# Optimization experiments

Measured on AMD Instinct MI355X. Metric: run time of the kernel, lower is better.

Reference implementation:

```python
import jax, jax.numpy as jnp
import numpy as np


def setup_inputs() -> dict:
    key = jax.random.key(0)
    k1, k2, k3 = jax.random.split(key, 3)
    N, E, D = 100000, 3200000, 32  # neurons, total edges (fan-in sum), feature dim
    src = jax.random.normal(k1, (N, D), dtype=jnp.float32)
    gather_idx = jax.random.randint(k2, (E,), 0, N, dtype=jnp.int32)
    # repeat_interleave(arange(N), repeats) is nondecreasing -> sorted segment ids
    segment_ids = jnp.sort(jax.random.randint(k3, (E,), 0, N, dtype=jnp.int32))
    return {"src": src, "gather_idx": gather_idx, "segment_ids": segment_ids, "num_segments": N}


def reference(src, gather_idx, segment_ids, num_segments):
    # gather neuron input values: [E, D]
    gathered = src[gather_idx]
    # scatter_mean over variable-length groups (segment mean)
    sums = jax.ops.segment_sum(gathered, segment_ids, num_segments=num_segments,
                               indices_are_sorted=True)
    counts = jax.ops.segment_sum(jnp.ones((gathered.shape[0],), dtype=src.dtype),
                                 segment_ids, num_segments=num_segments,
                                 indices_are_sorted=True)
    return sums / jnp.maximum(counts, 1.0)[:, None]
```

## Files before the change

kernel.cpp:

```cpp
#include <hip/hip_runtime.h>
#include <hip/hip_fp16.h>


constexpr int D = 32;
constexpr int GSZ = 4;
constexpr int BLOCK = 256;
constexpr int SEGS_PER_BLOCK = BLOCK / GSZ;

typedef _Float16 half8 __attribute__((ext_vector_type(8)));

__global__ __launch_bounds__(BLOCK) void prep_kernel(
    const float* __restrict__ src,
    const int*   __restrict__ segid,
    int*         __restrict__ start,
    _Float16*    __restrict__ hsrc,
    int E, int N, int total)
{
    const int e = blockIdx.x * BLOCK + threadIdx.x;

    if (e <= E) {
        int s, p;
        if (e == E) { s = N; p = segid[E - 1]; }
        else        { s = segid[e]; p = (e == 0) ? -1 : segid[e - 1]; }
        for (int n = p + 1; n <= s; ++n) start[n] = e;
    }

    const int i = e * 8;
    if (i < total) {
        const float4 a = *(const float4*)(src + i);
        const float4 b = *(const float4*)(src + i + 4);
        half8 h;
        h[0] = (_Float16)a.x; h[1] = (_Float16)a.y;
        h[2] = (_Float16)a.z; h[3] = (_Float16)a.w;
        h[4] = (_Float16)b.x; h[5] = (_Float16)b.y;
        h[6] = (_Float16)b.z; h[7] = (_Float16)b.w;
        *(half8*)(hsrc + i) = h;
    }
}

__global__ __launch_bounds__(BLOCK) void AggregationLayer_53051436040325_kernel(
    const _Float16* __restrict__ hsrc,
    const int*      __restrict__ gidx,
    const int*      __restrict__ start,
    float*          __restrict__ out,
    int N)
{
    const int n   = blockIdx.x * SEGS_PER_BLOCK + (threadIdx.x >> 2);
    const int sub = threadIdx.x & (GSZ - 1);
    if (n >= N) return;

    const int lo = start[n];
    const int hi = start[n + 1];

    const _Float16* sp = hsrc + sub * 8;

    float acc[8];
#pragma unroll
    for (int j = 0; j < 8; ++j) acc[j] = 0.f;

    int e = lo;
    for (; e + 8 <= hi; e += 8) {
        int g[8];
#pragma unroll
        for (int k = 0; k < 8; ++k) g[k] = gidx[e + k];
        half8 v[8];
#pragma unroll
        for (int k = 0; k < 8; ++k) v[k] = *(const half8*)(sp + (size_t)g[k] * D);
#pragma unroll
        for (int k = 0; k < 8; ++k)
#pragma unroll
            for (int j = 0; j < 8; ++j) acc[j] += (float)v[k][j];
    }
    for (; e < hi; ++e) {
        const half8 v = *(const half8*)(sp + (size_t)gidx[e] * D);
#pragma unroll
        for (int j = 0; j < 8; ++j) acc[j] += (float)v[j];
    }

    const int c = hi - lo;
    const float inv = 1.f / (float)(c > 0 ? c : 1);
    float4 r0, r1;
    r0.x = acc[0] * inv; r0.y = acc[1] * inv; r0.z = acc[2] * inv; r0.w = acc[3] * inv;
    r1.x = acc[4] * inv; r1.y = acc[5] * inv; r1.z = acc[6] * inv; r1.w = acc[7] * inv;
    float* op = out + (size_t)n * D + sub * 8;
    *(float4*)(op)     = r0;
    *(float4*)(op + 4) = r1;
}

extern "C" void kernel_launch(void* const* d_in, const int* in_sizes, int n_in,
                              void* d_out, int out_size, void* d_ws, size_t ws_size,
                              hipStream_t stream) {
    const float* src   = (const float*)d_in[0];
    const int*   gidx  = (const int*)d_in[1];
    const int*   segid = (const int*)d_in[2];
    const int E = in_sizes[1];
    const int N = in_sizes[0] / D;
    const int total = N * D;

    int*      start = (int*)d_ws;
    _Float16* hsrc  = (_Float16*)((char*)d_ws + ((size_t)(N + 1) * sizeof(int) + 255 & ~(size_t)255));

    float* out = (float*)d_out;

    const int blocksA = (E + 1 + BLOCK - 1) / BLOCK;
    prep_kernel<<<blocksA, BLOCK, 0, stream>>>(src, segid, start, hsrc, E, N, total);

    const int blocksB = (N + SEGS_PER_BLOCK - 1) / SEGS_PER_BLOCK;
    AggregationLayer_53051436040325_kernel<<<blocksB, BLOCK, 0, stream>>>(hsrc, gidx, start, out, N);
}
```

Before: 124.7 us.

## Split half-precision feature table into two column halves pinned to XCD groups

The fp16 copy of src is split into two tables, one per half of the 32 features. Aggregation blocks are assigned so that XCDs 0-3 gather only from half A and XCDs 4-7 only from half B. The goal is for each XCD's L2 to cache a smaller working set (about 3.2 MB instead of 6.4 MB), which should raise the gather hit rate. In exchange, the segment index array gidx and the start offsets are read twice, and each thread fetches a single 16-byte chunk per edge instead of sharing a row across four threads.

```diff
diff --git a/kernel.cpp b/kernel.cpp
--- a/kernel.cpp
+++ b/kernel.cpp
@@ -3,7 +3,8 @@
 
 
 constexpr int D = 32;
-constexpr int GSZ = 4;
+constexpr int HD = 16;
+constexpr int GSZ = 2;
 constexpr int BLOCK = 256;
 constexpr int SEGS_PER_BLOCK = BLOCK / GSZ;
 
@@ -13,46 +14,60 @@
     const float* __restrict__ src,
     const int*   __restrict__ segid,
     int*         __restrict__ start,
-    _Float16*    __restrict__ hsrc,
-    int E, int N, int total)
+    _Float16*    __restrict__ hsrcA,
+    _Float16*    __restrict__ hsrcB,
+    int E, int N)
 {
-    const int e = blockIdx.x * BLOCK + threadIdx.x;
+    const int t = blockIdx.x * BLOCK + threadIdx.x;
 
-    if (e <= E) {
+    if (t <= E) {
         int s, p;
-        if (e == E) { s = N; p = segid[E - 1]; }
-        else        { s = segid[e]; p = (e == 0) ? -1 : segid[e - 1]; }
-        for (int n = p + 1; n <= s; ++n) start[n] = e;
+        if (t == E) { s = N; p = segid[E - 1]; }
+        else        { s = segid[t]; p = (t == 0) ? -1 : segid[t - 1]; }
+        for (int n = p + 1; n <= s; ++n) start[n] = t;
     }
 
-    const int i = e * 8;
-    if (i < total) {
-        const float4 a = *(const float4*)(src + i);
-        const float4 b = *(const float4*)(src + i + 4);
-        half8 h;
-        h[0] = (_Float16)a.x; h[1] = (_Float16)a.y;
-        h[2] = (_Float16)a.z; h[3] = (_Float16)a.w;
-        h[4] = (_Float16)b.x; h[5] = (_Float16)b.y;
-        h[6] = (_Float16)b.z; h[7] = (_Float16)b.w;
-        *(half8*)(hsrc + i) = h;
+    if (t < 2 * N) {
+        const int  row  = (t < N) ? t : t - N;
+        const int  hoff = (t < N) ? 0 : HD;
+        _Float16*  dst  = (t < N) ? hsrcA : hsrcB;
+        const float* sp = src + (size_t)row * D + hoff;
+        const float4 a = *(const float4*)(sp);
+        const float4 b = *(const float4*)(sp + 4);
+        const float4 c = *(const float4*)(sp + 8);
+        const float4 d = *(const float4*)(sp + 12);
+        half8 h0, h1;
+        h0[0] = (_Float16)a.x; h0[1] = (_Float16)a.y; h0[2] = (_Float16)a.z; h0[3] = (_Float16)a.w;
+        h0[4] = (_Float16)b.x; h0[5] = (_Float16)b.y; h0[6] = (_Float16)b.z; h0[7] = (_Float16)b.w;
+        h1[0] = (_Float16)c.x; h1[1] = (_Float16)c.y; h1[2] = (_Float16)c.z; h1[3] = (_Float16)c.w;
+        h1[4] = (_Float16)d.x; h1[5] = (_Float16)d.y; h1[6] = (_Float16)d.z; h1[7] = (_Float16)d.w;
+        *(half8*)(dst + (size_t)row * HD)     = h0;
+        *(half8*)(dst + (size_t)row * HD + 8) = h1;
     }
 }
 
 __global__ __launch_bounds__(BLOCK) void AggregationLayer_53051436040325_kernel(
-    const _Float16* __restrict__ hsrc,
+    const _Float16* __restrict__ hsrcA,
+    const _Float16* __restrict__ hsrcB,
     const int*      __restrict__ gidx,
     const int*      __restrict__ start,
     float*          __restrict__ out,
-    int N)
+    int N, int nblkHalf)
 {
-    const int n   = blockIdx.x * SEGS_PER_BLOCK + (threadIdx.x >> 2);
-    const int sub = threadIdx.x & (GSZ - 1);
+    const int bid  = blockIdx.x;
+    const int xcd  = bid & 7;
+    const int hsel = xcd >> 2;
+    const int wblk = (bid >> 3) * 4 + (xcd & 3);
+    if (wblk >= nblkHalf) return;
+
+    const int n   = wblk * SEGS_PER_BLOCK + (threadIdx.x >> 1);
+    const int sub = threadIdx.x & 1;
     if (n >= N) return;
 
     const int lo = start[n];
     const int hi = start[n + 1];
 
-    const _Float16* sp = hsrc + sub * 8;
+    const _Float16* sp = (hsel ? hsrcB : hsrcA) + sub * 8;
 
     float acc[8];
 #pragma unroll
@@ -65,14 +80,14 @@
         for (int k = 0; k < 8; ++k) g[k] = gidx[e + k];
         half8 v[8];
 #pragma unroll
-        for (int k = 0; k < 8; ++k) v[k] = *(const half8*)(sp + (size_t)g[k] * D);
+        for (int k = 0; k < 8; ++k) v[k] = *(const half8*)(sp + (size_t)g[k] * HD);
 #pragma unroll
         for (int k = 0; k < 8; ++k)
 #pragma unroll
             for (int j = 0; j < 8; ++j) acc[j] += (float)v[k][j];
     }
     for (; e < hi; ++e) {
-        const half8 v = *(const half8*)(sp + (size_t)gidx[e] * D);
+        const half8 v = *(const half8*)(sp + (size_t)gidx[e] * HD);
 #pragma unroll
         for (int j = 0; j < 8; ++j) acc[j] += (float)v[j];
     }
@@ -82,7 +97,7 @@
     float4 r0, r1;
     r0.x = acc[0] * inv; r0.y = acc[1] * inv; r0.z = acc[2] * inv; r0.w = acc[3] * inv;
     r1.x = acc[4] * inv; r1.y = acc[5] * inv; r1.z = acc[6] * inv; r1.w = acc[7] * inv;
-    float* op = out + (size_t)n * D + sub * 8;
+    float* op = out + (size_t)n * D + hsel * HD + sub * 8;
     *(float4*)(op)     = r0;
     *(float4*)(op + 4) = r1;
 }
@@ -95,16 +110,22 @@
     const int*   segid = (const int*)d_in[2];
     const int E = in_sizes[1];
     const int N = in_sizes[0] / D;
-    const int total = N * D;
 
-    int*      start = (int*)d_ws;
-    _Float16* hsrc  = (_Float16*)((char*)d_ws + ((size_t)(N + 1) * sizeof(int) + 255 & ~(size_t)255));
+    char* ws = (char*)d_ws;
+    int* start = (int*)ws;
+    size_t off = ((size_t)(N + 1) * sizeof(int) + 255) & ~(size_t)255;
+    _Float16* hsrcA = (_Float16*)(ws + off);
+    off += ((size_t)N * HD * sizeof(_Float16) + 255) & ~(size_t)255;
+    _Float16* hsrcB = (_Float16*)(ws + off);
 
     float* out = (float*)d_out;
 
-    const int blocksA = (E + 1 + BLOCK - 1) / BLOCK;
-    prep_kernel<<<blocksA, BLOCK, 0, stream>>>(src, segid, start, hsrc, E, N, total);
+    const int threadsA = (E + 1 > 2 * N) ? (E + 1) : (2 * N);
+    const int blocksA = (threadsA + BLOCK - 1) / BLOCK;
+    prep_kernel<<<blocksA, BLOCK, 0, stream>>>(src, segid, start, hsrcA, hsrcB, E, N);
 
-    const int blocksB = (N + SEGS_PER_BLOCK - 1) / SEGS_PER_BLOCK;
-    AggregationLayer_53051436040325_kernel<<<blocksB, BLOCK, 0, stream>>>(hsrc, gidx, start, out, N);
+    const int nblkHalf = (N + SEGS_PER_BLOCK - 1) / SEGS_PER_BLOCK;
+    const int blocksB  = ((2 * nblkHalf + 7) / 8) * 8;
+    AggregationLayer_53051436040325_kernel<<<blocksB, BLOCK, 0, stream>>>(
+        hsrcA, hsrcB, gidx, start, out, N, nblkHalf);
 }
```

Result: slower. 140.4 us (+12.6%).
